# Kernel optimization log

Hardware: AMD Instinct MI355X
Metric: run time of the kernel (lower is better)

Reference implementation:

```python
import jax, jax.numpy as jnp
import numpy as np
import math

N_S = 4096
N_T = 4096
R = 0.05
SIGMA = 0.2
K = 100.0
T = 1.0
S_MAX = 300.0
B = 100.0
ALPHA_STR = 30.0
CHI = 6.0
LAMBDA_PDE = 1.0
LAMBDA_BC = 10.0
LAMBDA_TC = 10.0
HUBER_DELTA = 0.01
ALPHA = 2.0 * R / SIGMA ** 2            # 2r/sigma^2
TAU_MAX = 0.5 * SIGMA ** 2 * T
DU = 1.0 / (N_S - 1)                     # dS_norm for the S-stencils
DT_NORM = TAU_MAX / (N_T - 1)            # dt_norm for the t-stencil


def _solve_depressed_cubic(Q):
    # Faithful port of CubicStretching._solve_depressed_cubic (hyperbolic root formula).
    p = CHI
    q = CHI * Q
    sp = math.sqrt(p)
    arg = abs(q) / (2.0 * p * sp / (3.0 * math.sqrt(3.0)))
    arg = max(1.0, arg)
    c = 2.0 * sp * math.cosh(math.acosh(arg) / 3.0)
    return -c if q >= 0 else c


C1 = _solve_depressed_cubic((B - 0.0) / ALPHA_STR)
C2 = _solve_depressed_cubic((B - S_MAX) / ALPHA_STR)


def _stretch_metrics(u):
    # CubicStretching.compute_metrics: S(u), dS/du, d2S/du2.
    L = C2 * u + C1 * (1.0 - u)
    dL = C2 - C1
    S = B + ALPHA_STR * (L ** 3 / CHI + L)
    dS = ALPHA_STR * dL * (0.5 * L ** 2 + 1.0)
    d2S = ALPHA_STR * dL ** 2 * L
    return S, dS, d2S


def setup_inputs() -> dict:
    key = jax.random.key(0)
    V_norm = 0.1 * jax.random.normal(key, (1, 1, N_S, N_T), dtype=jnp.float32)
    return {"V_norm": V_norm}


def reference(V_norm):
    # u-grid along S (axis 2), t-grid along time (axis 3)
    u = jnp.linspace(0.0, 1.0, N_S, dtype=jnp.float32)[None, None, :, None]  # [1,1,N_S,1]
    t = jnp.linspace(0.0, 1.0, N_T, dtype=jnp.float32)                       # [N_T]

    S_phys, S_u, S_uu = _stretch_metrics(u)
    S_norm = S_phys / S_MAX       # stretched physical coordinate, normalized
    S_u_n = S_u / S_MAX
    S_uu_n = S_uu / S_MAX

    # FD stencils: (3,1) central diff / second diff along S, (1,3) central diff along t,
    # all with replicate padding (= torch padding_mode='replicate').
    Vp = jnp.pad(V_norm, ((0, 0), (0, 0), (1, 1), (0, 0)), mode='edge')
    V_u = (Vp[:, :, 2:, :] - Vp[:, :, :-2, :]) / (2.0 * DU)
    V_uu = (Vp[:, :, 2:, :] - 2.0 * V_norm + Vp[:, :, :-2, :]) / DU ** 2
    Vt = jnp.pad(V_norm, ((0, 0), (0, 0), (0, 0), (1, 1)), mode='edge')
    V_t = (Vt[:, :, :, 2:] - Vt[:, :, :, :-2]) / (2.0 * DT_NORM)

    # Chain rule from uniform u to stretched S
    V_S = V_u / S_u_n
    V_SS = (V_uu * S_u_n - V_u * S_uu_n) / S_u_n ** 3
    V_SS = jnp.clip(V_SS, -100.0, 100.0)

    residual = V_t - S_norm ** 2 * V_SS - ALPHA * S_norm * V_S + ALPHA * V_norm
    # interior mask = relu(1 - S0 - Smax - T - t0) == strict interior of the grid
    n_int = (N_S - 2) * (N_T - 2)
    pde_loss = jnp.sum(residual[:, :, 1:-1, 1:-1] ** 2) / n_int

    # far-field BC at S = S_max (row N_S-1): call option -> 1 - K exp(-r(1-t))/S_max
    bc_target = 1.0 - K * jnp.exp(-R * (1.0 - t)) / S_MAX
    loss_Smax = jnp.sum((V_norm[0, 0, -1, :] - bc_target) ** 2) / N_T

    # terminal condition at t = T (col N_t-1): softplus payoff on the UNIFORM u grid
    # (forward rebinds S_norm = self.S_grid_norm before calling terminal_payoff)
    payoff = jax.nn.softplus(50.0 * (u[0, 0, :, 0] - K / S_MAX)) / 50.0
    diff_T = V_norm[0, 0, :, -1] - payoff
    abs_d = jnp.abs(diff_T)
    loss_T = jnp.sum(jnp.where(abs_d < HUBER_DELTA,
                               0.5 * diff_T ** 2,
                               HUBER_DELTA * (abs_d - 0.5 * HUBER_DELTA))) / N_S

    total = LAMBDA_PDE * pde_loss + LAMBDA_BC * loss_Smax + LAMBDA_TC * loss_T
    return total
```

## Files before the change

### kernel.cpp

```cpp
#include <hip/hip_runtime.h>
#include <math.h>

#define NS 4096
#define NT 4096

__device__ __forceinline__ double block_reduce(double v, int tid) {
    #pragma unroll
    for (int off = 32; off > 0; off >>= 1)
        v += __shfl_down(v, off, 64);
    __shared__ double lds[4];
    const int lane = tid & 63, wv = tid >> 6;
    if (lane == 0) lds[wv] = v;
    __syncthreads();
    return lds[0] + lds[1] + lds[2] + lds[3];
}

__global__ __launch_bounds__(256) void bs_main(const float* __restrict__ V,
                                               double* __restrict__ part,
                                               double C1, double C2) {
    const int i   = blockIdx.x;
    const int tid = threadIdx.x;

    const double DU = 1.0 / (double)(NS - 1);
    const double u  = (double)i * DU;
    const double L  = C2 * u + C1 * (1.0 - u);
    const double dL = C2 - C1;
    const double S   = 100.0 + 30.0 * (L * L * L / 6.0 + L);
    const double dS  = 30.0 * dL * (0.5 * L * L + 1.0);
    const double d2S = 30.0 * dL * dL * L;

    const float Sn     = (float)(S   / 300.0);
    const float Sun    = (float)(dS  / 300.0);
    const float Suun   = (float)(d2S / 300.0);
    const float invSun  = 1.0f / Sun;
    const float invSun3 = invSun * invSun * invSun;
    const float Sn2 = Sn * Sn;
    const float AL  = 2.5f;
    const float ASn = AL * Sn;

    const float INV2DU = 2047.5f;
    const float INVDU2 = 16769025.0f;
    const float INV2DT = 102375.0f;

    const float* __restrict__ rowc = V + (size_t)i * NT;
    const bool inti = (i >= 1) && (i <= NS - 2);

    double pde = 0.0, bc = 0.0, tc = 0.0;

    #pragma unroll
    for (int s = 0; s < 4; ++s) {
        const int j0 = (tid + 256 * s) * 4;
        const float4 c = *(const float4*)(rowc + j0);
        const float cc[4] = {c.x, c.y, c.z, c.w};

        if (inti) {
            const float4 up4 = *(const float4*)(rowc - NT + j0);
            const float4 dn4 = *(const float4*)(rowc + NT + j0);
            const float uu[4] = {up4.x, up4.y, up4.z, up4.w};
            const float dd[4] = {dn4.x, dn4.y, dn4.z, dn4.w};
            const float lf = (j0 > 0)      ? rowc[j0 - 1] : 0.0f;
            const float rt = (j0 + 4 < NT) ? rowc[j0 + 4] : 0.0f;

            #pragma unroll
            for (int k = 0; k < 4; ++k) {
                const int j = j0 + k;
                if (j >= 1 && j <= NT - 2) {
                    const float cm = (k == 0) ? lf : cc[k - 1];
                    const float cp = (k == 3) ? rt : cc[k + 1];
                    const float Vu  = (dd[k] - uu[k]) * INV2DU;
                    const float Vuu = (dd[k] - 2.0f * cc[k] + uu[k]) * INVDU2;
                    const float Vt  = (cp - cm) * INV2DT;
                    const float VS  = Vu * invSun;
                    float VSS = (Vuu * Sun - Vu * Suun) * invSun3;
                    VSS = fminf(fmaxf(VSS, -100.0f), 100.0f);
                    const float r = Vt - Sn2 * VSS - ASn * VS + AL * cc[k];
                    pde += (double)(r * r);
                }
            }
        }

        if (i == NS - 1) {
            #pragma unroll
            for (int k = 0; k < 4; ++k) {
                const int j = j0 + k;
                const float t   = (float)j * (1.0f / (float)(NT - 1));
                const float tgt = 1.0f - (100.0f / 300.0f) * expf(-0.05f * (1.0f - t));
                const float d   = cc[k] - tgt;
                bc += (double)(d * d);
            }
        }

        if (j0 + 4 == NT) {
            const float ui = (float)u;
            const float x  = 50.0f * (ui - 100.0f / 300.0f);
            const float sp = fmaxf(x, 0.0f) + log1pf(expf(-fabsf(x)));
            const float payoff = sp * (1.0f / 50.0f);
            const float d  = c.w - payoff;
            const float ad = fabsf(d);
            const float h  = (ad < 0.01f) ? 0.5f * d * d : 0.01f * (ad - 0.005f);
            tc += (double)h;
        }
    }

    const double n_int = (double)(NS - 2) * (double)(NT - 2);
    double contrib = pde * (1.0 / n_int)
                   + bc  * (10.0 / (double)NT)
                   + tc  * (10.0 / (double)NS);

    contrib = block_reduce(contrib, tid);
    if (tid == 0) part[i] = contrib;
}

__global__ __launch_bounds__(256) void bs_final(const double* __restrict__ part,
                                                float* __restrict__ out) {
    const int tid = threadIdx.x;
    double s = 0.0;
    for (int idx = tid; idx < NS; idx += 256) s += part[idx];
    s = block_reduce(s, tid);
    if (tid == 0) out[0] = (float)s;
}

static double cubic_root_host(double Q) {
    const double p = 6.0;
    const double q = p * Q;
    const double sp = sqrt(p);
    double arg = fabs(q) / (2.0 * p * sp / (3.0 * sqrt(3.0)));
    if (arg < 1.0) arg = 1.0;
    const double c = 2.0 * sp * cosh(acosh(arg) / 3.0);
    return (q >= 0.0) ? -c : c;
}

extern "C" void kernel_launch(void* const* d_in, const int* in_sizes, int n_in,
                              void* d_out, int out_size, void* d_ws, size_t ws_size,
                              hipStream_t stream) {
    const float* V  = (const float*)d_in[0];
    float* out      = (float*)d_out;
    double* part    = (double*)d_ws;

    const double C1 = cubic_root_host((100.0 - 0.0)   / 30.0);
    const double C2 = cubic_root_host((100.0 - 300.0) / 30.0);

    bs_main <<<NS, 256, 0, stream>>>(V, part, C1, C2);
    bs_final<<<1,  256, 0, stream>>>(part, out);
}
```

Before: 110.8 us.

## Process four rows per block with register-rolling row reuse and float accumulation

Each block now handles four consecutive rows, with each thread owning 16 contiguous columns. Neighbouring rows are kept in registers and rotated, so every row is loaded about once instead of three times. The per-element double accumulation becomes a float partial sum per row that is converted to double once. The grid is a quarter of its former size, so there are fewer blocks to hide latency and more registers per thread.

```diff
diff --git a/kernel.cpp b/kernel.cpp
--- a/kernel.cpp
+++ b/kernel.cpp
@@ -3,6 +3,8 @@
 
 #define NS 4096
 #define NT 4096
+#define RPB 4
+#define NBLK (NS / RPB)
 
 __device__ __forceinline__ double block_reduce(double v, int tid) {
     #pragma unroll
@@ -15,91 +17,104 @@
     return lds[0] + lds[1] + lds[2] + lds[3];
 }
 
+__device__ __forceinline__ void load16(const float* __restrict__ p, float* d) {
+    const float4 x0 = *(const float4*)(p);
+    const float4 x1 = *(const float4*)(p + 4);
+    const float4 x2 = *(const float4*)(p + 8);
+    const float4 x3 = *(const float4*)(p + 12);
+    d[0]=x0.x; d[1]=x0.y; d[2]=x0.z;  d[3]=x0.w;
+    d[4]=x1.x; d[5]=x1.y; d[6]=x1.z;  d[7]=x1.w;
+    d[8]=x2.x; d[9]=x2.y; d[10]=x2.z; d[11]=x2.w;
+    d[12]=x3.x;d[13]=x3.y;d[14]=x3.z; d[15]=x3.w;
+}
+
 __global__ __launch_bounds__(256) void bs_main(const float* __restrict__ V,
                                                double* __restrict__ part,
                                                double C1, double C2) {
-    const int i   = blockIdx.x;
     const int tid = threadIdx.x;
+    const int r0  = blockIdx.x * RPB;
+    const int j0  = tid * 16;
 
     const double DU = 1.0 / (double)(NS - 1);
-    const double u  = (double)i * DU;
-    const double L  = C2 * u + C1 * (1.0 - u);
     const double dL = C2 - C1;
-    const double S   = 100.0 + 30.0 * (L * L * L / 6.0 + L);
-    const double dS  = 30.0 * dL * (0.5 * L * L + 1.0);
-    const double d2S = 30.0 * dL * dL * L;
-
-    const float Sn     = (float)(S   / 300.0);
-    const float Sun    = (float)(dS  / 300.0);
-    const float Suun   = (float)(d2S / 300.0);
-    const float invSun  = 1.0f / Sun;
-    const float invSun3 = invSun * invSun * invSun;
-    const float Sn2 = Sn * Sn;
-    const float AL  = 2.5f;
-    const float ASn = AL * Sn;
 
     const float INV2DU = 2047.5f;
     const float INVDU2 = 16769025.0f;
     const float INV2DT = 102375.0f;
+    const float AL     = 2.5f;
 
-    const float* __restrict__ rowc = V + (size_t)i * NT;
-    const bool inti = (i >= 1) && (i <= NS - 2);
+    float a[16], b[16], c[16];
+    const int rm = (r0 > 0) ? r0 - 1 : 0;
+    load16(V + (size_t)rm * NT + j0, a);
+    load16(V + (size_t)r0 * NT + j0, b);
 
     double pde = 0.0, bc = 0.0, tc = 0.0;
 
     #pragma unroll
-    for (int s = 0; s < 4; ++s) {
-        const int j0 = (tid + 256 * s) * 4;
-        const float4 c = *(const float4*)(rowc + j0);
-        const float cc[4] = {c.x, c.y, c.z, c.w};
+    for (int rr = 0; rr < RPB; ++rr) {
+        const int r  = r0 + rr;
+        const int rn = (r + 1 < NS) ? r + 1 : NS - 1;
+        load16(V + (size_t)rn * NT + j0, c);
 
-        if (inti) {
-            const float4 up4 = *(const float4*)(rowc - NT + j0);
-            const float4 dn4 = *(const float4*)(rowc + NT + j0);
-            const float uu[4] = {up4.x, up4.y, up4.z, up4.w};
-            const float dd[4] = {dn4.x, dn4.y, dn4.z, dn4.w};
-            const float lf = (j0 > 0)      ? rowc[j0 - 1] : 0.0f;
-            const float rt = (j0 + 4 < NT) ? rowc[j0 + 4] : 0.0f;
+        const double u   = (double)r * DU;
+        const double L   = C2 * u + C1 * (1.0 - u);
+        const double S   = 100.0 + 30.0 * (L * L * L / 6.0 + L);
+        const double dS  = 30.0 * dL * (0.5 * L * L + 1.0);
+        const double d2S = 30.0 * dL * dL * L;
+        const float Sn   = (float)(S   / 300.0);
+        const float Sun  = (float)(dS  / 300.0);
+        const float Suun = (float)(d2S / 300.0);
+        const float invSun  = 1.0f / Sun;
+        const float invSun3 = invSun * invSun * invSun;
+        const float Sn2 = Sn * Sn;
+        const float ASn = AL * Sn;
 
+        if (r >= 1 && r <= NS - 2) {
+            const float lf = (j0 > 0)       ? V[(size_t)r * NT + j0 - 1]  : 0.0f;
+            const float rt = (j0 + 16 < NT) ? V[(size_t)r * NT + j0 + 16] : 0.0f;
+
+            float pf = 0.0f;
             #pragma unroll
-            for (int k = 0; k < 4; ++k) {
+            for (int k = 0; k < 16; ++k) {
                 const int j = j0 + k;
                 if (j >= 1 && j <= NT - 2) {
-                    const float cm = (k == 0) ? lf : cc[k - 1];
-                    const float cp = (k == 3) ? rt : cc[k + 1];
-                    const float Vu  = (dd[k] - uu[k]) * INV2DU;
-                    const float Vuu = (dd[k] - 2.0f * cc[k] + uu[k]) * INVDU2;
+                    const float cm = (k == 0)  ? lf : b[k - 1];
+                    const float cp = (k == 15) ? rt : b[k + 1];
+                    const float Vu  = (c[k] - a[k]) * INV2DU;
+                    const float Vuu = (c[k] - 2.0f * b[k] + a[k]) * INVDU2;
                     const float Vt  = (cp - cm) * INV2DT;
                     const float VS  = Vu * invSun;
                     float VSS = (Vuu * Sun - Vu * Suun) * invSun3;
                     VSS = fminf(fmaxf(VSS, -100.0f), 100.0f);
-                    const float r = Vt - Sn2 * VSS - ASn * VS + AL * cc[k];
-                    pde += (double)(r * r);
+                    const float res = Vt - Sn2 * VSS - ASn * VS + AL * b[k];
+                    pf += res * res;
                 }
             }
+            pde += (double)pf;
         }
 
-        if (i == NS - 1) {
+        if (r == NS - 1) {
             #pragma unroll
-            for (int k = 0; k < 4; ++k) {
-                const int j = j0 + k;
-                const float t   = (float)j * (1.0f / (float)(NT - 1));
+            for (int k = 0; k < 16; ++k) {
+                const float t   = (float)(j0 + k) * (1.0f / (float)(NT - 1));
                 const float tgt = 1.0f - (100.0f / 300.0f) * expf(-0.05f * (1.0f - t));
-                const float d   = cc[k] - tgt;
+                const float d   = b[k] - tgt;
                 bc += (double)(d * d);
             }
         }
 
-        if (j0 + 4 == NT) {
+        if (tid == 255) {
             const float ui = (float)u;
             const float x  = 50.0f * (ui - 100.0f / 300.0f);
             const float sp = fmaxf(x, 0.0f) + log1pf(expf(-fabsf(x)));
             const float payoff = sp * (1.0f / 50.0f);
-            const float d  = c.w - payoff;
+            const float d  = b[15] - payoff;
             const float ad = fabsf(d);
-            const float h  = (ad < 0.01f) ? 0.5f * d * d : 0.01f * (ad - 0.005f);
-            tc += (double)h;
+            tc += (double)((ad < 0.01f) ? 0.5f * d * d : 0.01f * (ad - 0.005f));
         }
+
+        #pragma unroll
+        for (int k = 0; k < 16; ++k) { a[k] = b[k]; b[k] = c[k]; }
     }
 
     const double n_int = (double)(NS - 2) * (double)(NT - 2);
@@ -108,14 +123,14 @@
                    + tc  * (10.0 / (double)NS);
 
     contrib = block_reduce(contrib, tid);
-    if (tid == 0) part[i] = contrib;
+    if (tid == 0) part[blockIdx.x] = contrib;
 }
 
 __global__ __launch_bounds__(256) void bs_final(const double* __restrict__ part,
                                                 float* __restrict__ out) {
     const int tid = threadIdx.x;
     double s = 0.0;
-    for (int idx = tid; idx < NS; idx += 256) s += part[idx];
+    for (int idx = tid; idx < NBLK; idx += 256) s += part[idx];
     s = block_reduce(s, tid);
     if (tid == 0) out[0] = (float)s;
 }
@@ -140,6 +155,6 @@
     const double C1 = cubic_root_host((100.0 - 0.0)   / 30.0);
     const double C2 = cubic_root_host((100.0 - 300.0) / 30.0);
 
-    bs_main <<<NS, 256, 0, stream>>>(V, part, C1, C2);
-    bs_final<<<1,  256, 0, stream>>>(part, out);
+    bs_main <<<NBLK, 256, 0, stream>>>(V, part, C1, C2);
+    bs_final<<<1,    256, 0, stream>>>(part, out);
 }
```

New measurement: 100.2 us. -9.5%, faster.
